# Kernel optimization log

Hardware: AMD Instinct MI355X
Metric: run time of the kernel (lower is better)

The kernel has to match this reference:

```python
import jax, jax.numpy as jnp
import numpy as np
from jax import lax

SAMPLE_RATE = 44100.0

def _shelf_coeffs(gain_db, fc, q, sr, high):
    # RBJ cookbook shelf biquad; high=True -> high_shelf, else low_shelf
    A = 10.0 ** (gain_db / 40.0)
    w0 = 2.0 * jnp.pi * (fc / sr)
    alpha = jnp.sin(w0) / (2.0 * q)
    c = jnp.cos(w0)
    sA = jnp.sqrt(A)
    sgn = 1.0 if high else -1.0
    b0 = A * (A + 1 + sgn * (A - 1) * c + 2 * sA * alpha)
    b1 = -2.0 * sgn * A * (A - 1 + sgn * (A + 1) * c)
    b2 = A * (A + 1 + sgn * (A - 1) * c - 2 * sA * alpha)
    a0 = A + 1 - sgn * (A - 1) * c + 2 * sA * alpha
    a1 = 2.0 * sgn * (A - 1 - sgn * (A + 1) * c)
    a2 = A + 1 - sgn * (A - 1) * c - 2 * sA * alpha
    b = jnp.stack([b0, b1, b2]) / a0
    a = jnp.stack([a0, a1, a2]) / a0
    return b, a

def _peaking_coeffs(gain_db, fc, q, sr):
    A = 10.0 ** (gain_db / 40.0)
    w0 = 2.0 * jnp.pi * (fc / sr)
    alpha = jnp.sin(w0) / (2.0 * q)
    c = jnp.cos(w0)
    b0 = 1 + alpha * A
    b1 = -2.0 * c
    b2 = 1 - alpha * A
    a0 = 1 + alpha / A
    a1 = -2.0 * c
    a2 = 1 - alpha / A
    b = jnp.stack([b0, b1, b2]) / a0
    a = jnp.stack([a0, a1, a2]) / a0
    return b, a

def _biquad_lfilter(b, a, x):
    # scipy.signal.lfilter with zero initial conditions, transposed DF-II.
    # x: (chs, T); state s: (chs, 2)
    b0, b1, b2 = b[0], b[1], b[2]
    a1, a2 = a[1], a[2]
    def step(s, xn):  # xn: (chs,)
        s1, s2 = s[:, 0], s[:, 1]
        yn = b0 * xn + s1
        s1n = b1 * xn - a1 * yn + s2
        s2n = b2 * xn - a2 * yn
        return jnp.stack([s1n, s2n], axis=1), yn
    s0 = jnp.zeros((x.shape[0], 2), x.dtype)
    _, y = lax.scan(step, s0, x.T)  # y: (T, chs)
    return y.T

def setup_inputs() -> dict:
    key = jax.random.key(0)
    x = jax.random.normal(key, (8, 2097152), dtype=jnp.float32)
    # rows: [low_shelf, band1, band2, band3, high_shelf]; cols: [gain_db, cutoff_hz, Q]
    eq_params = jnp.array([
        [3.0, 100.0, 0.9],
        [-2.5, 400.0, 1.2],
        [4.0, 1000.0, 2.0],
        [-5.0, 4000.0, 0.7],
        [2.5, 12000.0, 0.707],
    ], dtype=jnp.float32)
    return {"x": x, "eq_params": eq_params}

def reference(x, eq_params):
    sr = SAMPLE_RATE
    # low shelf
    b, a = _shelf_coeffs(eq_params[0, 0], eq_params[0, 1], eq_params[0, 2], sr, high=False)
    y = _biquad_lfilter(b, a, x)
    # 3 peaking bands
    for i in range(1, 4):
        b, a = _peaking_coeffs(eq_params[i, 0], eq_params[i, 1], eq_params[i, 2], sr)
        y = _biquad_lfilter(b, a, y)
    # high shelf
    b, a = _shelf_coeffs(eq_params[4, 0], eq_params[4, 1], eq_params[4, 2], sr, high=True)
    y = _biquad_lfilter(b, a, y)
    return y.astype(jnp.float32)
```

## Files before the change

### kernel.cpp

```cpp
#include <hip/hip_runtime.h>

#define SRATE 44100.0
#define L_CHUNK 64
#define SAMPLES_PER_CH 2097152
#define CHUNKS_PER_CH 32768
#define NCH 8
#define TOTAL_CHUNKS 262144
#define CPB 256
#define NBLK 1024
#define BLK_PER_CH 128
#define NWIN 4
#define WIN 16
#define STRIDE 17

#ifndef M_PI
#define M_PI 3.14159265358979323846
#endif

struct CoefD { double b0, b1, b2, a1, a2; };

__device__ void cascade_step_d(const CoefD* cf, double* s, double x) {
    double u = x;
    #pragma unroll
    for (int i = 0; i < 5; i++) {
        double y   = cf[i].b0 * u + s[2*i];
        double s1n = cf[i].b1 * u - cf[i].a1 * y + s[2*i+1];
        double s2n = cf[i].b2 * u - cf[i].a2 * y;
        s[2*i]   = s1n;
        s[2*i+1] = s2n;
        u = y;
    }
}

__global__ __launch_bounds__(128) void k0_setup(const float* __restrict__ eqp,
                                                float* __restrict__ coef_f,
                                                float* __restrict__ mats_f) {
    __shared__ CoefD cf[5];
    __shared__ double M[100];
    int t = threadIdx.x;

    if (t == 0) {
        for (int i = 0; i < 5; i++) {
            double g  = (double)eqp[i*3 + 0];
            double fc = (double)eqp[i*3 + 1];
            double q  = (double)eqp[i*3 + 2];
            double A  = pow(10.0, g / 40.0);
            double w0 = 2.0 * M_PI * (fc / SRATE);
            double al = sin(w0) / (2.0 * q);
            double c  = cos(w0);
            double b0, b1, b2, a0, a1, a2;
            if (i == 0 || i == 4) {
                double sgn = (i == 4) ? 1.0 : -1.0;
                double sA = sqrt(A);
                b0 = A * ((A + 1.0) + sgn * (A - 1.0) * c + 2.0 * sA * al);
                b1 = -2.0 * sgn * A * ((A - 1.0) + sgn * (A + 1.0) * c);
                b2 = A * ((A + 1.0) + sgn * (A - 1.0) * c - 2.0 * sA * al);
                a0 = (A + 1.0) - sgn * (A - 1.0) * c + 2.0 * sA * al;
                a1 = 2.0 * sgn * ((A - 1.0) - sgn * (A + 1.0) * c);
                a2 = (A + 1.0) - sgn * (A - 1.0) * c - 2.0 * sA * al;
            } else {
                b0 = 1.0 + al * A; b1 = -2.0 * c; b2 = 1.0 - al * A;
                a0 = 1.0 + al / A; a1 = -2.0 * c; a2 = 1.0 - al / A;
            }
            cf[i].b0 = b0 / a0; cf[i].b1 = b1 / a0; cf[i].b2 = b2 / a0;
            cf[i].a1 = a1 / a0; cf[i].a2 = a2 / a0;
            coef_f[i*5 + 0] = (float)(b0 / a0);
            coef_f[i*5 + 1] = (float)(b1 / a0);
            coef_f[i*5 + 2] = (float)(b2 / a0);
            coef_f[i*5 + 3] = (float)(a1 / a0);
            coef_f[i*5 + 4] = (float)(a2 / a0);
        }
    }
    __syncthreads();

    if (t < 10) {
        double s[10];
        for (int k = 0; k < 10; k++) s[k] = (k == t) ? 1.0 : 0.0;
        cascade_step_d(cf, s, 0.0);
        for (int r = 0; r < 10; r++) M[r*10 + t] = s[r];
    }
    __syncthreads();

    for (int k = 1; k <= 20; k++) {
        double val = 0.0;
        if (t < 100) {
            int r = t / 10, c = t % 10;
            for (int j = 0; j < 10; j++) val += M[r*10 + j] * M[j*10 + c];
        }
        __syncthreads();
        if (t < 100) {
            M[t] = val;
            if (k >= 6 && k <= 13)  mats_f[(k-6)*100 + t]        = (float)val;
            if (k >= 14)            mats_f[800 + (k-14)*100 + t] = (float)val;
        }
        __syncthreads();
    }
}

__global__ __launch_bounds__(256, 4) void k1_partial(const float* __restrict__ x,
                                                     const float* __restrict__ coef,
                                                     const float* __restrict__ mats_f,
                                                     float* __restrict__ ibuf,
                                                     float* __restrict__ abuf) {
    __shared__ float smem[CPB * STRIDE];
    __shared__ float Mds[800];
    int t = threadIdx.x, b = blockIdx.x;

    const float4* x4 = (const float4*)x;
    const size_t base4 = (size_t)b * (CPB * L_CHUNK / 4);
    const int cb = t >> 2, q = t & 3;

    float4 rr[4];
    #pragma unroll
    for (int k = 0; k < 4; k++)
        rr[k] = x4[base4 + (size_t)(cb + 64*k) * (L_CHUNK/4) + q];

    for (int i = t; i < 800; i += 256) Mds[i] = mats_f[i];

    float cb0[5], cb1[5], cb2[5], ca1[5], ca2[5];
    #pragma unroll
    for (int i = 0; i < 5; i++) {
        cb0[i] = coef[i*5+0]; cb1[i] = coef[i*5+1]; cb2[i] = coef[i*5+2];
        ca1[i] = coef[i*5+3]; ca2[i] = coef[i*5+4];
    }

    #pragma unroll
    for (int k = 0; k < 4; k++) {
        int o = (cb + 64*k) * STRIDE + q*4;
        smem[o+0] = rr[k].x; smem[o+1] = rr[k].y;
        smem[o+2] = rr[k].z; smem[o+3] = rr[k].w;
    }
    __syncthreads();

    float s[10];
    #pragma unroll
    for (int k = 0; k < 10; k++) s[k] = 0.0f;

    for (int w = 0; w < NWIN; w++) {
        if (w + 1 < NWIN) {
            #pragma unroll
            for (int k = 0; k < 4; k++)
                rr[k] = x4[base4 + (size_t)(cb + 64*k) * (L_CHUNK/4) + (w+1)*4 + q];
        }
        const float* cur = smem + t * STRIDE;
        #pragma unroll
        for (int i = 0; i < WIN; i++) {
            float u = cur[i];
            #pragma unroll
            for (int st = 0; st < 5; st++) {
                float y  = fmaf(cb0[st], u, s[2*st]);
                float t1 = fmaf(cb1[st], u, s[2*st+1]);
                s[2*st+1] = fmaf(-ca2[st], y, cb2[st] * u);
                s[2*st]   = fmaf(-ca1[st], y, t1);
                u = y;
            }
        }
        __syncthreads();
        if (w + 1 < NWIN) {
            #pragma unroll
            for (int k = 0; k < 4; k++) {
                int o = (cb + 64*k) * STRIDE + q*4;
                smem[o+0] = rr[k].x; smem[o+1] = rr[k].y;
                smem[o+2] = rr[k].z; smem[o+3] = rr[k].w;
            }
            __syncthreads();
        }
    }

    float v[10];
    #pragma unroll
    for (int r = 0; r < 10; r++) { v[r] = s[r]; smem[t*11 + r] = v[r]; }
    __syncthreads();

    for (int d = 0; d < 8; d++) {
        float nv[10];
        bool act = (t >= (1 << d));
        if (act) {
            int src = t - (1 << d);
            #pragma unroll
            for (int r = 0; r < 10; r++) {
                float acc = v[r];
                #pragma unroll
                for (int k = 0; k < 10; k++)
                    acc = fmaf(Mds[d*100 + r*10 + k], smem[src*11 + k], acc);
                nv[r] = acc;
            }
        }
        __syncthreads();
        if (act) {
            #pragma unroll
            for (int r = 0; r < 10; r++) { v[r] = nv[r]; smem[t*11 + r] = nv[r]; }
        }
        __syncthreads();
    }

    #pragma unroll
    for (int r = 0; r < 10; r++)
        ibuf[(size_t)b * 2560 + r * 256 + t] = (t > 0) ? smem[(t-1)*11 + r] : 0.0f;
    if (t == 255) {
        #pragma unroll
        for (int r = 0; r < 10; r++) abuf[b * 10 + r] = v[r];
    }
}

__global__ __launch_bounds__(1024) void k2b_scan(const float* __restrict__ mats_f,
                                                 const float* __restrict__ abuf,
                                                 float* __restrict__ bbuf) {
    __shared__ float Qds[700];
    __shared__ float buf[1024][11];
    int t = threadIdx.x;
    int i = t & (BLK_PER_CH - 1);

    for (int k = t; k < 700; k += 1024) Qds[k] = mats_f[800 + k];

    float v[10];
    #pragma unroll
    for (int r = 0; r < 10; r++) { v[r] = abuf[t * 10 + r]; buf[t][r] = v[r]; }
    __syncthreads();

    for (int e = 0; e < 7; e++) {
        float nv[10];
        bool act = (i >= (1 << e));
        if (act) {
            int src = t - (1 << e);
            #pragma unroll
            for (int r = 0; r < 10; r++) {
                float acc = v[r];
                #pragma unroll
                for (int k = 0; k < 10; k++)
                    acc = fmaf(Qds[e*100 + r*10 + k], buf[src][k], acc);
                nv[r] = acc;
            }
        }
        __syncthreads();
        if (act) {
            #pragma unroll
            for (int r = 0; r < 10; r++) { v[r] = nv[r]; buf[t][r] = nv[r]; }
        }
        __syncthreads();
    }
    #pragma unroll
    for (int r = 0; r < 10; r++)
        bbuf[t * 10 + r] = (i > 0) ? buf[t-1][r] : 0.0f;
}

__global__ __launch_bounds__(256, 4) void k3_final(const float* __restrict__ x,
                                                   const float* __restrict__ coef,
                                                   const float* __restrict__ mats_f,
                                                   const float* __restrict__ ibuf,
                                                   const float* __restrict__ bbuf,
                                                   float* __restrict__ out) {
    __shared__ float inb[CPB * STRIDE];
    __shared__ float outb[CPB * STRIDE];
    __shared__ float Mds[800];
    int t = threadIdx.x, b = blockIdx.x;

    const float4* x4 = (const float4*)x;
    float4* o4 = (float4*)out;
    const size_t base4 = (size_t)b * (CPB * L_CHUNK / 4);
    const int cb = t >> 2, q = t & 3;

    float4 rr[4];
    #pragma unroll
    for (int k = 0; k < 4; k++)
        rr[k] = x4[base4 + (size_t)(cb + 64*k) * (L_CHUNK/4) + q];

    for (int i = t; i < 800; i += 256) Mds[i] = mats_f[i];

    float cb0[5], cb1[5], cb2[5], ca1[5], ca2[5];
    #pragma unroll
    for (int i = 0; i < 5; i++) {
        cb0[i] = coef[i*5+0]; cb1[i] = coef[i*5+1]; cb2[i] = coef[i*5+2];
        ca1[i] = coef[i*5+3]; ca2[i] = coef[i*5+4];
    }

    float s[10];
    #pragma unroll
    for (int r = 0; r < 10; r++)
        s[r] = ibuf[(size_t)b * 2560 + r * 256 + t];
    float v[10];
    #pragma unroll
    for (int r = 0; r < 10; r++) v[r] = bbuf[b * 10 + r];

    #pragma unroll
    for (int k = 0; k < 4; k++) {
        int o = (cb + 64*k) * STRIDE + q*4;
        inb[o+0] = rr[k].x; inb[o+1] = rr[k].y;
        inb[o+2] = rr[k].z; inb[o+3] = rr[k].w;
    }
    __syncthreads();

    for (int d = 0; d < 8; d++) {
        float wv[10];
        #pragma unroll
        for (int r = 0; r < 10; r++) {
            float acc = 0.0f;
            #pragma unroll
            for (int k = 0; k < 10; k++)
                acc = fmaf(Mds[d*100 + r*10 + k], v[k], acc);
            wv[r] = acc;
        }
        bool bit = (t >> d) & 1;
        #pragma unroll
        for (int r = 0; r < 10; r++) v[r] = bit ? wv[r] : v[r];
    }
    #pragma unroll
    for (int r = 0; r < 10; r++) s[r] += v[r];

    for (int w = 0; w < NWIN; w++) {
        if (w + 1 < NWIN) {
            #pragma unroll
            for (int k = 0; k < 4; k++)
                rr[k] = x4[base4 + (size_t)(cb + 64*k) * (L_CHUNK/4) + (w+1)*4 + q];
        }
        const float* cur = inb + t * STRIDE;
        float* orow = outb + t * STRIDE;
        #pragma unroll
        for (int i = 0; i < WIN; i++) {
            float u = cur[i];
            #pragma unroll
            for (int st = 0; st < 5; st++) {
                float y  = fmaf(cb0[st], u, s[2*st]);
                float t1 = fmaf(cb1[st], u, s[2*st+1]);
                s[2*st+1] = fmaf(-ca2[st], y, cb2[st] * u);
                s[2*st]   = fmaf(-ca1[st], y, t1);
                u = y;
            }
            orow[i] = u;
        }
        __syncthreads();

        #pragma unroll
        for (int k = 0; k < 4; k++) {
            int o = (cb + 64*k) * STRIDE + q*4;
            float4 ov = make_float4(outb[o+0], outb[o+1], outb[o+2], outb[o+3]);
            o4[base4 + (size_t)(cb + 64*k) * (L_CHUNK/4) + (size_t)w*4 + q] = ov;
        }
        if (w + 1 < NWIN) {
            #pragma unroll
            for (int k = 0; k < 4; k++) {
                int o = (cb + 64*k) * STRIDE + q*4;
                inb[o+0] = rr[k].x; inb[o+1] = rr[k].y;
                inb[o+2] = rr[k].z; inb[o+3] = rr[k].w;
            }
            __syncthreads();
        }
    }
}

extern "C" void kernel_launch(void* const* d_in, const int* in_sizes, int n_in,
                              void* d_out, int out_size, void* d_ws, size_t ws_size,
                              hipStream_t stream) {
    const float* x   = (const float*)d_in[0];
    const float* eqp = (const float*)d_in[1];
    float* out = (float*)d_out;
    char* ws = (char*)d_ws;

    float* coef_f = (float*)ws;
    float* mats_f = (float*)(ws + 256);
    float* abuf   = (float*)(ws + 8192);
    float* bbuf   = (float*)(ws + 49152);
    float* ibuf   = (float*)(ws + 98304);

    hipLaunchKernelGGL(k0_setup, dim3(1), dim3(128), 0, stream, eqp, coef_f, mats_f);
    hipLaunchKernelGGL(k1_partial, dim3(NBLK), dim3(256), 0, stream,
                       x, coef_f, mats_f, ibuf, abuf);
    hipLaunchKernelGGL(k2b_scan, dim3(1), dim3(1024), 0, stream, mats_f, abuf, bbuf);
    hipLaunchKernelGGL(k3_final, dim3(NBLK), dim3(256), 0, stream,
                       x, coef_f, mats_f, ibuf, bbuf, out);
}
```

Measured before the change: 186.9 us.

## Fuse partial, scan and final passes into one kernel with decoupled lookback flags

Merges the three-kernel chunked IIR scan into one kernel. Blocks publish their aggregate state with release flags, and later blocks in the same channel spin on those flags, then run an in-block scan over their predecessors' aggregates. Each thread now keeps its 64 input samples in registers, so input is read once per pass and the ibuf round-trip and the separate scan launch go away. The risk is a deadlock if earlier blocks are not resident, since this relies on block scheduling order, along with more register pressure and redundant per-block scan work.

```diff
diff --git a/kernel.cpp b/kernel.cpp
--- a/kernel.cpp
+++ b/kernel.cpp
@@ -34,10 +34,13 @@
 
 __global__ __launch_bounds__(128) void k0_setup(const float* __restrict__ eqp,
                                                 float* __restrict__ coef_f,
-                                                float* __restrict__ mats_f) {
+                                                float* __restrict__ mats_f,
+                                                unsigned* __restrict__ flags) {
     __shared__ CoefD cf[5];
     __shared__ double M[100];
     int t = threadIdx.x;
+
+    for (int i = t; i < NBLK; i += 128) flags[i] = 0u;
 
     if (t == 0) {
         for (int i = 0; i < 5; i++) {
@@ -97,25 +100,34 @@
     }
 }
 
-__global__ __launch_bounds__(256, 4) void k1_partial(const float* __restrict__ x,
-                                                     const float* __restrict__ coef,
-                                                     const float* __restrict__ mats_f,
-                                                     float* __restrict__ ibuf,
-                                                     float* __restrict__ abuf) {
+__device__ __forceinline__ float cascade5(float u, float* s,
+                                          const float* b0, const float* b1,
+                                          const float* b2, const float* a1,
+                                          const float* a2) {
+    #pragma unroll
+    for (int st = 0; st < 5; st++) {
+        float y  = fmaf(b0[st], u, s[2*st]);
+        float t1 = fmaf(b1[st], u, s[2*st+1]);
+        s[2*st+1] = fmaf(-a2[st], y, b2[st] * u);
+        s[2*st]   = fmaf(-a1[st], y, t1);
+        u = y;
+    }
+    return u;
+}
+
+__global__ __launch_bounds__(256, 4) void k_main(const float* __restrict__ x,
+                                                 const float* __restrict__ coef,
+                                                 const float* __restrict__ mats_f,
+                                                 float* __restrict__ abuf,
+                                                 unsigned* __restrict__ flags,
+                                                 float* __restrict__ out) {
     __shared__ float smem[CPB * STRIDE];
-    __shared__ float Mds[800];
-    int t = threadIdx.x, b = blockIdx.x;
-
-    const float4* x4 = (const float4*)x;
-    const size_t base4 = (size_t)b * (CPB * L_CHUNK / 4);
-    const int cb = t >> 2, q = t & 3;
-
-    float4 rr[4];
-    #pragma unroll
-    for (int k = 0; k < 4; k++)
-        rr[k] = x4[base4 + (size_t)(cb + 64*k) * (L_CHUNK/4) + q];
-
-    for (int i = t; i < 800; i += 256) Mds[i] = mats_f[i];
+    __shared__ float Mds[1500];
+    const int t = threadIdx.x, b = blockIdx.x;
+    const int ch     = b >> 7;
+    const int ch_blk = b & (BLK_PER_CH - 1);
+
+    for (int i = t; i < 1500; i += 256) Mds[i] = mats_f[i];
 
     float cb0[5], cb1[5], cb2[5], ca1[5], ca2[5];
     #pragma unroll
@@ -124,52 +136,23 @@
         ca1[i] = coef[i*5+3]; ca2[i] = coef[i*5+4];
     }
 
-    #pragma unroll
-    for (int k = 0; k < 4; k++) {
-        int o = (cb + 64*k) * STRIDE + q*4;
-        smem[o+0] = rr[k].x; smem[o+1] = rr[k].y;
-        smem[o+2] = rr[k].z; smem[o+3] = rr[k].w;
-    }
-    __syncthreads();
-
+    const float4* x4 = (const float4*)x;
+    const size_t tb4 = (size_t)b * 4096 + (size_t)t * 16;
     float s[10];
     #pragma unroll
     for (int k = 0; k < 10; k++) s[k] = 0.0f;
-
-    for (int w = 0; w < NWIN; w++) {
-        if (w + 1 < NWIN) {
-            #pragma unroll
-            for (int k = 0; k < 4; k++)
-                rr[k] = x4[base4 + (size_t)(cb + 64*k) * (L_CHUNK/4) + (w+1)*4 + q];
-        }
-        const float* cur = smem + t * STRIDE;
-        #pragma unroll
-        for (int i = 0; i < WIN; i++) {
-            float u = cur[i];
-            #pragma unroll
-            for (int st = 0; st < 5; st++) {
-                float y  = fmaf(cb0[st], u, s[2*st]);
-                float t1 = fmaf(cb1[st], u, s[2*st+1]);
-                s[2*st+1] = fmaf(-ca2[st], y, cb2[st] * u);
-                s[2*st]   = fmaf(-ca1[st], y, t1);
-                u = y;
-            }
-        }
-        __syncthreads();
-        if (w + 1 < NWIN) {
-            #pragma unroll
-            for (int k = 0; k < 4; k++) {
-                int o = (cb + 64*k) * STRIDE + q*4;
-                smem[o+0] = rr[k].x; smem[o+1] = rr[k].y;
-                smem[o+2] = rr[k].z; smem[o+3] = rr[k].w;
-            }
-            __syncthreads();
-        }
-    }
-
-    float v[10];
-    #pragma unroll
-    for (int r = 0; r < 10; r++) { v[r] = s[r]; smem[t*11 + r] = v[r]; }
+    #pragma unroll
+    for (int k = 0; k < 16; k++) {
+        float4 xv = x4[tb4 + k];
+        cascade5(xv.x, s, cb0, cb1, cb2, ca1, ca2);
+        cascade5(xv.y, s, cb0, cb1, cb2, ca1, ca2);
+        cascade5(xv.z, s, cb0, cb1, cb2, ca1, ca2);
+        cascade5(xv.w, s, cb0, cb1, cb2, ca1, ca2);
+    }
+
+    __syncthreads();
+    #pragma unroll
+    for (int r = 0; r < 10; r++) smem[t*11 + r] = s[r];
     __syncthreads();
 
     for (int d = 0; d < 8; d++) {
@@ -179,7 +162,7 @@
             int src = t - (1 << d);
             #pragma unroll
             for (int r = 0; r < 10; r++) {
-                float acc = v[r];
+                float acc = s[r];
                 #pragma unroll
                 for (int k = 0; k < 10; k++)
                     acc = fmaf(Mds[d*100 + r*10 + k], smem[src*11 + k], acc);
@@ -189,107 +172,79 @@
         __syncthreads();
         if (act) {
             #pragma unroll
-            for (int r = 0; r < 10; r++) { v[r] = nv[r]; smem[t*11 + r] = nv[r]; }
-        }
-        __syncthreads();
-    }
-
-    #pragma unroll
-    for (int r = 0; r < 10; r++)
-        ibuf[(size_t)b * 2560 + r * 256 + t] = (t > 0) ? smem[(t-1)*11 + r] : 0.0f;
+            for (int r = 0; r < 10; r++) { s[r] = nv[r]; smem[t*11 + r] = nv[r]; }
+        }
+        __syncthreads();
+    }
+
+    float p[10];
+    #pragma unroll
+    for (int r = 0; r < 10; r++) p[r] = (t > 0) ? smem[(t-1)*11 + r] : 0.0f;
+
     if (t == 255) {
         #pragma unroll
-        for (int r = 0; r < 10; r++) abuf[b * 10 + r] = v[r];
-    }
-}
-
-__global__ __launch_bounds__(1024) void k2b_scan(const float* __restrict__ mats_f,
-                                                 const float* __restrict__ abuf,
-                                                 float* __restrict__ bbuf) {
-    __shared__ float Qds[700];
-    __shared__ float buf[1024][11];
-    int t = threadIdx.x;
-    int i = t & (BLK_PER_CH - 1);
-
-    for (int k = t; k < 700; k += 1024) Qds[k] = mats_f[800 + k];
-
-    float v[10];
-    #pragma unroll
-    for (int r = 0; r < 10; r++) { v[r] = abuf[t * 10 + r]; buf[t][r] = v[r]; }
+        for (int r = 0; r < 10; r++)
+            __hip_atomic_store(&abuf[b*10 + r], s[r],
+                               __ATOMIC_RELAXED, __HIP_MEMORY_SCOPE_AGENT);
+        __hip_atomic_store(&flags[b], 1u,
+                           __ATOMIC_RELEASE, __HIP_MEMORY_SCOPE_AGENT);
+    }
+
+    if (t < ch_blk) {
+        const unsigned* fp = &flags[ch * BLK_PER_CH + t];
+        while (__hip_atomic_load(fp, __ATOMIC_ACQUIRE,
+                                 __HIP_MEMORY_SCOPE_AGENT) == 0u) {
+            __builtin_amdgcn_s_sleep(8);
+        }
+    }
+    __syncthreads();
+
+    float v2[10];
+    if (t < ch_blk) {
+        const float* ap = &abuf[(ch * BLK_PER_CH + t) * 10];
+        #pragma unroll
+        for (int r = 0; r < 10; r++) {
+            v2[r] = __hip_atomic_load(&ap[r], __ATOMIC_RELAXED,
+                                      __HIP_MEMORY_SCOPE_AGENT);
+            smem[t*11 + r] = v2[r];
+        }
+    }
     __syncthreads();
 
     for (int e = 0; e < 7; e++) {
+        if ((1 << e) >= ch_blk) break;
         float nv[10];
-        bool act = (i >= (1 << e));
+        bool act = (t < ch_blk) && (t >= (1 << e));
         if (act) {
             int src = t - (1 << e);
             #pragma unroll
             for (int r = 0; r < 10; r++) {
-                float acc = v[r];
+                float acc = v2[r];
                 #pragma unroll
                 for (int k = 0; k < 10; k++)
-                    acc = fmaf(Qds[e*100 + r*10 + k], buf[src][k], acc);
+                    acc = fmaf(Mds[800 + e*100 + r*10 + k], smem[src*11 + k], acc);
                 nv[r] = acc;
             }
         }
         __syncthreads();
         if (act) {
             #pragma unroll
-            for (int r = 0; r < 10; r++) { v[r] = nv[r]; buf[t][r] = nv[r]; }
-        }
-        __syncthreads();
-    }
+            for (int r = 0; r < 10; r++) { v2[r] = nv[r]; smem[t*11 + r] = nv[r]; }
+        }
+        __syncthreads();
+    }
+
+    float w[10];
     #pragma unroll
     for (int r = 0; r < 10; r++)
-        bbuf[t * 10 + r] = (i > 0) ? buf[t-1][r] : 0.0f;
-}
-
-__global__ __launch_bounds__(256, 4) void k3_final(const float* __restrict__ x,
-                                                   const float* __restrict__ coef,
-                                                   const float* __restrict__ mats_f,
-                                                   const float* __restrict__ ibuf,
-                                                   const float* __restrict__ bbuf,
-                                                   float* __restrict__ out) {
-    __shared__ float inb[CPB * STRIDE];
-    __shared__ float outb[CPB * STRIDE];
-    __shared__ float Mds[800];
-    int t = threadIdx.x, b = blockIdx.x;
-
-    const float4* x4 = (const float4*)x;
-    float4* o4 = (float4*)out;
-    const size_t base4 = (size_t)b * (CPB * L_CHUNK / 4);
-    const int cb = t >> 2, q = t & 3;
-
-    float4 rr[4];
-    #pragma unroll
-    for (int k = 0; k < 4; k++)
-        rr[k] = x4[base4 + (size_t)(cb + 64*k) * (L_CHUNK/4) + q];
-
-    for (int i = t; i < 800; i += 256) Mds[i] = mats_f[i];
-
-    float cb0[5], cb1[5], cb2[5], ca1[5], ca2[5];
-    #pragma unroll
-    for (int i = 0; i < 5; i++) {
-        cb0[i] = coef[i*5+0]; cb1[i] = coef[i*5+1]; cb2[i] = coef[i*5+2];
-        ca1[i] = coef[i*5+3]; ca2[i] = coef[i*5+4];
-    }
-
-    float s[10];
-    #pragma unroll
-    for (int r = 0; r < 10; r++)
-        s[r] = ibuf[(size_t)b * 2560 + r * 256 + t];
-    float v[10];
-    #pragma unroll
-    for (int r = 0; r < 10; r++) v[r] = bbuf[b * 10 + r];
-
-    #pragma unroll
-    for (int k = 0; k < 4; k++) {
-        int o = (cb + 64*k) * STRIDE + q*4;
-        inb[o+0] = rr[k].x; inb[o+1] = rr[k].y;
-        inb[o+2] = rr[k].z; inb[o+3] = rr[k].w;
-    }
-    __syncthreads();
-
+        w[r] = (ch_blk > 0) ? smem[(ch_blk-1)*11 + r] : 0.0f;
+    __syncthreads();
+
+    float4 xr[16];
+    #pragma unroll
+    for (int k = 0; k < 16; k++) xr[k] = x4[tb4 + k];
+
+    #pragma unroll
     for (int d = 0; d < 8; d++) {
         float wv[10];
         #pragma unroll
@@ -297,54 +252,40 @@
             float acc = 0.0f;
             #pragma unroll
             for (int k = 0; k < 10; k++)
-                acc = fmaf(Mds[d*100 + r*10 + k], v[k], acc);
+                acc = fmaf(Mds[d*100 + r*10 + k], w[k], acc);
             wv[r] = acc;
         }
         bool bit = (t >> d) & 1;
         #pragma unroll
-        for (int r = 0; r < 10; r++) v[r] = bit ? wv[r] : v[r];
-    }
-    #pragma unroll
-    for (int r = 0; r < 10; r++) s[r] += v[r];
-
-    for (int w = 0; w < NWIN; w++) {
-        if (w + 1 < NWIN) {
-            #pragma unroll
-            for (int k = 0; k < 4; k++)
-                rr[k] = x4[base4 + (size_t)(cb + 64*k) * (L_CHUNK/4) + (w+1)*4 + q];
-        }
-        const float* cur = inb + t * STRIDE;
-        float* orow = outb + t * STRIDE;
-        #pragma unroll
-        for (int i = 0; i < WIN; i++) {
-            float u = cur[i];
-            #pragma unroll
-            for (int st = 0; st < 5; st++) {
-                float y  = fmaf(cb0[st], u, s[2*st]);
-                float t1 = fmaf(cb1[st], u, s[2*st+1]);
-                s[2*st+1] = fmaf(-ca2[st], y, cb2[st] * u);
-                s[2*st]   = fmaf(-ca1[st], y, t1);
-                u = y;
-            }
-            orow[i] = u;
-        }
-        __syncthreads();
-
+        for (int r = 0; r < 10; r++) w[r] = bit ? wv[r] : w[r];
+    }
+    #pragma unroll
+    for (int r = 0; r < 10; r++) s[r] = p[r] + w[r];
+
+    float4* o4 = (float4*)out;
+    const size_t base4 = (size_t)b * 4096;
+    const int cbi = t >> 2, q = t & 3;
+
+    #pragma unroll
+    for (int wnd = 0; wnd < NWIN; wnd++) {
+        float* orow = smem + t * STRIDE;
         #pragma unroll
         for (int k = 0; k < 4; k++) {
-            int o = (cb + 64*k) * STRIDE + q*4;
-            float4 ov = make_float4(outb[o+0], outb[o+1], outb[o+2], outb[o+3]);
-            o4[base4 + (size_t)(cb + 64*k) * (L_CHUNK/4) + (size_t)w*4 + q] = ov;
-        }
-        if (w + 1 < NWIN) {
-            #pragma unroll
-            for (int k = 0; k < 4; k++) {
-                int o = (cb + 64*k) * STRIDE + q*4;
-                inb[o+0] = rr[k].x; inb[o+1] = rr[k].y;
-                inb[o+2] = rr[k].z; inb[o+3] = rr[k].w;
-            }
-            __syncthreads();
-        }
+            const float4 xv = xr[wnd*4 + k];
+            orow[k*4+0] = cascade5(xv.x, s, cb0, cb1, cb2, ca1, ca2);
+            orow[k*4+1] = cascade5(xv.y, s, cb0, cb1, cb2, ca1, ca2);
+            orow[k*4+2] = cascade5(xv.z, s, cb0, cb1, cb2, ca1, ca2);
+            orow[k*4+3] = cascade5(xv.w, s, cb0, cb1, cb2, ca1, ca2);
+        }
+        __syncthreads();
+
+        #pragma unroll
+        for (int k = 0; k < 4; k++) {
+            int o = (cbi + 64*k) * STRIDE + q*4;
+            float4 ov = make_float4(smem[o+0], smem[o+1], smem[o+2], smem[o+3]);
+            o4[base4 + (size_t)(cbi + 64*k) * 16 + (size_t)wnd*4 + q] = ov;
+        }
+        __syncthreads();
     }
 }
 
@@ -356,16 +297,13 @@
     float* out = (float*)d_out;
     char* ws = (char*)d_ws;
 
-    float* coef_f = (float*)ws;
-    float* mats_f = (float*)(ws + 256);
-    float* abuf   = (float*)(ws + 8192);
-    float* bbuf   = (float*)(ws + 49152);
-    float* ibuf   = (float*)(ws + 98304);
-
-    hipLaunchKernelGGL(k0_setup, dim3(1), dim3(128), 0, stream, eqp, coef_f, mats_f);
-    hipLaunchKernelGGL(k1_partial, dim3(NBLK), dim3(256), 0, stream,
-                       x, coef_f, mats_f, ibuf, abuf);
-    hipLaunchKernelGGL(k2b_scan, dim3(1), dim3(1024), 0, stream, mats_f, abuf, bbuf);
-    hipLaunchKernelGGL(k3_final, dim3(NBLK), dim3(256), 0, stream,
-                       x, coef_f, mats_f, ibuf, bbuf, out);
-}
+    float*    coef_f = (float*)ws;
+    float*    mats_f = (float*)(ws + 256);
+    float*    abuf   = (float*)(ws + 8192);
+    unsigned* flags  = (unsigned*)(ws + 65536);
+
+    hipLaunchKernelGGL(k0_setup, dim3(1), dim3(128), 0, stream,
+                       eqp, coef_f, mats_f, flags);
+    hipLaunchKernelGGL(k_main, dim3(NBLK), dim3(256), 0, stream,
+                       x, coef_f, mats_f, abuf, flags, out);
+}
```

Measured after the change: 226.0 us. +20.9%, slower.
